# Optimization experiments

Measured on AMD Instinct MI355X. Metric: run time of the kernel, lower is better.

## Reference

```python
import jax, jax.numpy as jnp
import numpy as np

N_NODES = 50000


def _gcn_conv(x, src, dst, W, b, n):
    # PyG GCNConv: h = x @ W; symmetric normalization with self-loops; scatter-add; + bias
    h = x @ W
    deg = jax.ops.segment_sum(jnp.ones_like(dst, dtype=h.dtype), dst, num_segments=n)
    dinv = jax.lax.rsqrt(jnp.maximum(deg, 1.0))  # self-loops guarantee deg >= 1
    norm = dinv[src] * dinv[dst]                 # [E_total]
    msgs = h[src] * norm[:, None]                # gather + scale
    out = jax.ops.segment_sum(msgs, dst, num_segments=n)
    return out + b


def setup_inputs() -> dict:
    key = jax.random.key(0)
    k1, k2, k3, k4 = jax.random.split(key, 4)
    d, f = 128, 128
    x = jax.random.normal(k1, (N_NODES, d), dtype=jnp.float32)
    edge_index = jax.random.randint(k2, (2, 800000), 0, N_NODES, dtype=jnp.int64)
    W1 = jax.random.normal(k3, (d, f), dtype=jnp.float32) / np.sqrt(d)
    b1 = jnp.zeros((f,), dtype=jnp.float32)
    W2 = jax.random.normal(k4, (f, 1), dtype=jnp.float32) / np.sqrt(f)
    b2 = jnp.zeros((1,), dtype=jnp.float32)
    return {"x": x, "edge_index": edge_index, "W1": W1, "b1": b1, "W2": W2, "b2": b2}


def reference(x, edge_index, W1, b1, W2, b2):
    n = x.shape[0]
    loops = jnp.arange(n, dtype=edge_index.dtype)
    src = jnp.concatenate([edge_index[0], loops])
    dst = jnp.concatenate([edge_index[1], loops])
    h = _gcn_conv(x, src, dst, W1, b1, n)
    h = jax.nn.relu(h)
    out = _gcn_conv(h, src, dst, W2, b2, n)
    return out
```

## Files before the change

kernel.cpp:

```cpp
#include <hip/hip_runtime.h>
#include <hip/hip_fp16.h>

#define D 128
#define BINW 64
#define BINCAP 2048
#define SUBT 1568
#define LCAP 48

typedef _Float16 half8 __attribute__((ext_vector_type(8)));
typedef float float4v __attribute__((ext_vector_type(4)));

__global__ __launch_bounds__(256) void fused_bin_gemm_kernel(
    const float* __restrict__ x, const float* __restrict__ W,
    __half* __restrict__ h, const int* __restrict__ idx,
    int* __restrict__ binCount, unsigned* __restrict__ binned,
    int E, int nbin, int n, int SB) {
  __shared__ uint4 smem[2048];
  const int t = threadIdx.x;

  if (blockIdx.x < SB) {
    int*            hist  = (int*)smem;
    int*            cur   = hist + 800;
    unsigned*       recs  = (unsigned*)(cur + 800);
    unsigned short* dbins = (unsigned short*)(recs + SUBT);
    int*            isp   = (int*)(dbins + SUBT);

    for (int b = t; b < 800; b += 256) hist[b] = 0;
    if (t == 0) {
      int any = 0;
      for (int i = 0; i < 64; ++i) any |= idx[2 * i + 1];
      *isp = (any == 0) ? 1 : 0;
    }
    __syncthreads();
    const int is64 = *isp;
    const int lo = blockIdx.x * SUBT;
    const int hi = min(lo + SUBT, E);
    const int cnt_e = hi - lo;

    for (int e = lo + t; e < hi; e += 256) {
      int s, d;
      if (is64) { s = idx[2 * e]; d = idx[2 * (E + e)]; }
      else      { s = idx[e];     d = idx[E + e]; }
      const int li = e - lo;
      const int b = d >> 6;
      recs[li]  = (unsigned)s | ((unsigned)(d & 63) << 16);
      dbins[li] = (unsigned short)b;
      atomicAdd(&hist[b], 1);
    }
    __syncthreads();
    for (int b = t; b < nbin; b += 256) {
      int hv = hist[b];
      cur[b] = hv ? atomicAdd(&binCount[b], hv) : 0;
    }
    __syncthreads();
    for (int li = t; li < cnt_e; li += 256) {
      const int b = dbins[li];
      int pos = atomicAdd(&cur[b], 1);
      pos = min(pos, BINCAP - 1);
      binned[(size_t)b * BINCAP + pos] = recs[li];
    }
  } else {
    const int bid = blockIdx.x - SB;
    uint4 (*bfrag)[4][64] = (uint4(*)[4][64])smem;

    for (int e = t; e < 2048; e += 256) {
      const int nt = e >> 8;
      const int kk = (e >> 6) & 3;
      const int L  = e & 63;
      const int nn = nt * 16 + (L & 15);
      const int k0 = kk * 32 + (L >> 4) * 8;
      half8 v;
#pragma unroll
      for (int j = 0; j < 8; ++j) v[j] = (_Float16)W[(k0 + j) * D + nn];
      bfrag[nt][kk][L] = *(uint4*)&v;
    }
    __syncthreads();

    const int wave = t >> 6;
    const int lane = t & 63;
    const int r0 = bid * 64 + wave * 16;

    const int mrow = r0 + (lane & 15);
    const int mc = (mrow < n) ? mrow : (n - 1);
    half8 af[4];
#pragma unroll
    for (int kk = 0; kk < 4; ++kk) {
      const float* xp = x + (size_t)mc * D + kk * 32 + (lane >> 4) * 8;
      float4 lo4 = *(const float4*)xp;
      float4 hi4 = *(const float4*)(xp + 4);
      half8 v;
      v[0] = (_Float16)lo4.x; v[1] = (_Float16)lo4.y;
      v[2] = (_Float16)lo4.z; v[3] = (_Float16)lo4.w;
      v[4] = (_Float16)hi4.x; v[5] = (_Float16)hi4.y;
      v[6] = (_Float16)hi4.z; v[7] = (_Float16)hi4.w;
      af[kk] = v;
    }

    float4v acc[8];
#pragma unroll
    for (int nt = 0; nt < 8; ++nt) acc[nt] = (float4v){0.f, 0.f, 0.f, 0.f};

#pragma unroll
    for (int nt = 0; nt < 8; ++nt) {
      uint4 b0 = bfrag[nt][0][lane];
      uint4 b1 = bfrag[nt][1][lane];
      uint4 b2 = bfrag[nt][2][lane];
      uint4 b3 = bfrag[nt][3][lane];
      acc[nt] = __builtin_amdgcn_mfma_f32_16x16x32_f16(af[0], *(half8*)&b0, acc[nt], 0, 0, 0);
      acc[nt] = __builtin_amdgcn_mfma_f32_16x16x32_f16(af[1], *(half8*)&b1, acc[nt], 0, 0, 0);
      acc[nt] = __builtin_amdgcn_mfma_f32_16x16x32_f16(af[2], *(half8*)&b2, acc[nt], 0, 0, 0);
      acc[nt] = __builtin_amdgcn_mfma_f32_16x16x32_f16(af[3], *(half8*)&b3, acc[nt], 0, 0, 0);
    }

    __syncthreads();
    __half* hout = (__half*)smem;
    const int quad = lane >> 4;
    const int col  = lane & 15;
    const int rloc = wave * 16 + quad * 4;
#pragma unroll
    for (int r = 0; r < 4; ++r)
#pragma unroll
      for (int nt = 0; nt < 8; ++nt)
        hout[(rloc + r) * D + nt * 16 + col] = __float2half(acc[nt][r]);
    __syncthreads();

    const size_t rowbase = (size_t)bid * 64;
#pragma unroll
    for (int i = 0; i < 4; ++i) {
      const int elt = i * 256 + t;
      const int rr  = elt >> 4;
      if (rowbase + rr < (size_t)n)
        *(uint4*)(h + (rowbase + rr) * D + (elt & 15) * 8) = smem[elt];
    }
  }
}

__global__ __launch_bounds__(256) void sort_lists_kernel(const int* __restrict__ binCount,
                                                         const unsigned* __restrict__ binned,
                                                         unsigned short* __restrict__ lists,
                                                         int* __restrict__ cnt,
                                                         int n, int nbin) {
  __shared__ unsigned rec[BINCAP];
  __shared__ unsigned short srt[BINCAP];
  __shared__ int hist[BINW];
  __shared__ int scn[BINW];
  __shared__ int cur[BINW];
  const int t = threadIdx.x;
  const int b = blockIdx.x;
  int bc = binCount[b];
  if (bc > BINCAP) bc = BINCAP;
  const size_t gbase = (size_t)b * BINCAP;

  for (int i = t; i < bc; i += 256) rec[i] = binned[gbase + i];
  if (t < BINW) hist[t] = 0;
  __syncthreads();
  for (int i = t; i < bc; i += 256) atomicAdd(&hist[rec[i] >> 16], 1);
  __syncthreads();
  if (t < BINW) scn[t] = hist[t];
  __syncthreads();
  for (int off = 1; off < BINW; off <<= 1) {
    int u = 0;
    if (t < BINW && t >= off) u = scn[t - off];
    __syncthreads();
    if (t < BINW) scn[t] += u;
    __syncthreads();
  }
  if (t < BINW) cur[t] = scn[t] - hist[t];
  __syncthreads();
  for (int i = t; i < bc; i += 256) {
    unsigned r = rec[i];
    int pos = atomicAdd(&cur[r >> 16], 1);
    srt[pos] = (unsigned short)(r & 0xFFFFu);
  }
  __syncthreads();
  const int node0 = b * BINW;
  for (int i = t; i < BINW * LCAP; i += 256) {
    const int ln = i / LCAP;
    const int k  = i - ln * LCAP;
    const int node = node0 + ln;
    if (node < n) {
      const int deg = min(hist[ln], LCAP);
      if (k < deg) lists[(size_t)node * LCAP + k] = srt[scn[ln] - hist[ln] + k];
    }
  }
  const int node = node0 + t;
  if (t < BINW && node < n) cnt[node] = hist[t];
}

__device__ __forceinline__ void unpack8(uint4 p, float f[8]) {
  float2 t;
  t = __half22float2(*(__half2*)&p.x); f[0] = t.x; f[1] = t.y;
  t = __half22float2(*(__half2*)&p.y); f[2] = t.x; f[3] = t.y;
  t = __half22float2(*(__half2*)&p.z); f[4] = t.x; f[5] = t.y;
  t = __half22float2(*(__half2*)&p.w); f[6] = t.x; f[7] = t.y;
}

__global__ __launch_bounds__(256) void gather1_kernel(const __half* __restrict__ h,
                                                      const int* __restrict__ cnt,
                                                      const unsigned short* __restrict__ lists,
                                                      const float* __restrict__ b1,
                                                      const float* __restrict__ W2,
                                                      float* __restrict__ zw, int n) {
  const int node = blockIdx.x * 4 + (threadIdx.x >> 6);
  if (node >= n) return;
  const int lane = threadIdx.x & 63;
  const int q    = lane >> 4;
  const int fb   = (lane & 15) * 8;

  const unsigned short* lst = lists + (size_t)node * LCAP;
  const int  c   = cnt[node];
  const int  deg = min(c, LCAP);
  const float di = rsqrtf((float)(c + 1));
  float a[8] = {0.f, 0.f, 0.f, 0.f, 0.f, 0.f, 0.f, 0.f};
  if (q == 0) {
    uint4 p = *(const uint4*)(h + (size_t)node * D + fb);
    float f[8]; unpack8(p, f);
    float s2 = di * di;
#pragma unroll
    for (int k = 0; k < 8; ++k) a[k] = f[k] * s2;
  }

  for (int j = q; j < deg; j += 16) {
    const int j1 = j + 4, j2 = j + 8, j3 = j + 12;
    const bool v1 = j1 < deg, v2 = j2 < deg, v3 = j3 < deg;
    int s0 = lst[j];
    int s1 = v1 ? lst[j1] : s0;
    int s2 = v2 ? lst[j2] : s0;
    int s3 = v3 ? lst[j3] : s0;
    uint4 p0 = *(const uint4*)(h + (size_t)s0 * D + fb);
    uint4 p1 = *(const uint4*)(h + (size_t)s1 * D + fb);
    uint4 p2 = *(const uint4*)(h + (size_t)s2 * D + fb);
    uint4 p3 = *(const uint4*)(h + (size_t)s3 * D + fb);
    float w0 = di * rsqrtf((float)(cnt[s0] + 1));
    float w1 = v1 ? di * rsqrtf((float)(cnt[s1] + 1)) : 0.f;
    float w2 = v2 ? di * rsqrtf((float)(cnt[s2] + 1)) : 0.f;
    float w3 = v3 ? di * rsqrtf((float)(cnt[s3] + 1)) : 0.f;
    float f0[8], f1[8], f2[8], f3[8];
    unpack8(p0, f0); unpack8(p1, f1); unpack8(p2, f2); unpack8(p3, f3);
#pragma unroll
    for (int k = 0; k < 8; ++k) a[k] = fmaf(f0[k], w0, a[k]);
#pragma unroll
    for (int k = 0; k < 8; ++k) a[k] = fmaf(f1[k], w1, a[k]);
#pragma unroll
    for (int k = 0; k < 8; ++k) a[k] = fmaf(f2[k], w2, a[k]);
#pragma unroll
    for (int k = 0; k < 8; ++k) a[k] = fmaf(f3[k], w3, a[k]);
  }

#pragma unroll
  for (int k = 0; k < 8; ++k) {
    a[k] += __shfl_xor(a[k], 16, 64);
    a[k] += __shfl_xor(a[k], 32, 64);
  }

  float4 blo = *(const float4*)(b1 + fb);
  float4 bhi = *(const float4*)(b1 + fb + 4);
  float4 wlo = *(const float4*)(W2 + fb);
  float4 whi = *(const float4*)(W2 + fb + 4);
  float bb[8] = {blo.x, blo.y, blo.z, blo.w, bhi.x, bhi.y, bhi.z, bhi.w};
  float ww[8] = {wlo.x, wlo.y, wlo.z, wlo.w, whi.x, whi.y, whi.z, whi.w};
  float p = 0.f;
#pragma unroll
  for (int k = 0; k < 8; ++k) p += fmaxf(a[k] + bb[k], 0.f) * ww[k];
#pragma unroll
  for (int off = 8; off > 0; off >>= 1) p += __shfl_xor(p, off, 64);
  if (lane == 0) zw[node] = p * di;
}

__global__ __launch_bounds__(256) void gather2_kernel(const float* __restrict__ zw,
                                                      const int* __restrict__ cnt,
                                                      const unsigned short* __restrict__ lists,
                                                      const float* __restrict__ b2,
                                                      float* __restrict__ out, int n) {
  const int node = blockIdx.x * 64 + (threadIdx.x >> 2);
  if (node >= n) return;
  const int l = threadIdx.x & 3;
  const int c = cnt[node];
  const int deg = min(c, LCAP);
  const unsigned short* lst = lists + (size_t)node * LCAP;
  float s = (l == 0) ? zw[node] : 0.f;
  for (int j = l; j < deg; j += 4) s += zw[lst[j]];
  s += __shfl_xor(s, 1, 64);
  s += __shfl_xor(s, 2, 64);
  if (l == 0) out[node] = s * rsqrtf((float)(c + 1)) + b2[0];
}

extern "C" void kernel_launch(void* const* d_in, const int* in_sizes, int n_in,
                              void* d_out, int out_size, void* d_ws, size_t ws_size,
                              hipStream_t stream) {
  const float* x   = (const float*)d_in[0];
  const int*   idx = (const int*)d_in[1];
  const float* W1  = (const float*)d_in[2];
  const float* b1  = (const float*)d_in[3];
  const float* W2  = (const float*)d_in[4];
  const float* b2  = (const float*)d_in[5];
  float* out = (float*)d_out;

  const int n = in_sizes[0] / D;
  const int E = in_sizes[1] / 2;
  const int nbin = (n + BINW - 1) / BINW;

  char* ws = (char*)d_ws;
  size_t off = 0;
  auto carve = [&](size_t bytes) { char* p = ws + off; off += (bytes + 255) & ~(size_t)255; return p; };
  int*            binCount = (int*)carve((size_t)nbin * 4);
  unsigned*       binned   = (unsigned*)carve((size_t)nbin * BINCAP * 4);
  unsigned short* lists    = (unsigned short*)carve((size_t)n * LCAP * 2);
  int*            cnt      = (int*)carve((size_t)n * 4);
  __half*         h        = (__half*)carve((size_t)n * D * 2);
  float*          zw       = (float*)carve((size_t)n * 4);

  const int SB = (E + SUBT - 1) / SUBT;
  const int GB = (n + 63) / 64;

  hipMemsetAsync(binCount, 0, (size_t)nbin * 4, stream);
  fused_bin_gemm_kernel<<<SB + GB, 256, 0, stream>>>(x, W1, h, idx, binCount,
                                                     binned, E, nbin, n, SB);
  sort_lists_kernel<<<nbin, 256, 0, stream>>>(binCount, binned, lists, cnt, n, nbin);
  gather1_kernel<<<(n + 3) / 4, 256, 0, stream>>>(h, cnt, lists, b1, W2, zw, n);
  gather2_kernel<<<(n + 63) / 64, 256, 0, stream>>>(zw, cnt, lists, b2, out, n);
}
```

Before: 160.0 us.

## Switch to two-level binning with coarse 1024-node chunks and coalesced writes

Edges are first binned into 49 coarse chunks of 1024 destination nodes instead of 782 fine bins of 64. Each block locally sorts its records by chunk so it can write contiguous runs to global memory, replacing scattered per-edge writes. The sort kernel then has 16 blocks per chunk; each scans the whole chunk and keeps only records for its 64-node sub-bin. This cuts global atomics and scattered writes, but every chunk is read 16 times and the per-chunk capacity is fixed at 20480 (expected about 16400 edges), so overflow can drop edges.

```diff
diff --git a/kernel.cpp b/kernel.cpp
--- a/kernel.cpp
+++ b/kernel.cpp
@@ -2,6 +2,8 @@
 #include <hip/hip_fp16.h>
 
 #define D 128
+#define NC 64
+#define BINCAP2 20480
 #define BINW 64
 #define BINCAP 2048
 #define SUBT 1568
@@ -13,19 +15,24 @@
 __global__ __launch_bounds__(256) void fused_bin_gemm_kernel(
     const float* __restrict__ x, const float* __restrict__ W,
     __half* __restrict__ h, const int* __restrict__ idx,
-    int* __restrict__ binCount, unsigned* __restrict__ binned,
-    int E, int nbin, int n, int SB) {
+    int* __restrict__ binCount2, unsigned* __restrict__ binned,
+    int E, int nc, int n, int SB) {
   __shared__ uint4 smem[2048];
   const int t = threadIdx.x;
 
   if (blockIdx.x < SB) {
-    int*            hist  = (int*)smem;
-    int*            cur   = hist + 800;
-    unsigned*       recs  = (unsigned*)(cur + 800);
-    unsigned short* dbins = (unsigned short*)(recs + SUBT);
-    int*            isp   = (int*)(dbins + SUBT);
-
-    for (int b = t; b < 800; b += 256) hist[b] = 0;
+    int*           hist  = (int*)smem;
+    int*           scn   = hist + 64;
+    int*           lbase = scn + 64;
+    int*           cur   = lbase + 64;
+    int*           gbase = cur + 64;
+    unsigned*      recs  = (unsigned*)(gbase + 64);
+    unsigned*      srt   = recs + SUBT;
+    unsigned char* dbins = (unsigned char*)(srt + SUBT);
+    unsigned char* sbins = dbins + SUBT;
+    int*           isp   = (int*)(sbins + SUBT);
+
+    if (t < 64) hist[t] = 0;
     if (t == 0) {
       int any = 0;
       for (int i = 0; i < 64; ++i) any |= idx[2 * i + 1];
@@ -42,22 +49,39 @@
       if (is64) { s = idx[2 * e]; d = idx[2 * (E + e)]; }
       else      { s = idx[e];     d = idx[E + e]; }
       const int li = e - lo;
-      const int b = d >> 6;
-      recs[li]  = (unsigned)s | ((unsigned)(d & 63) << 16);
-      dbins[li] = (unsigned short)b;
+      const int b = d >> 10;
+      recs[li]  = (unsigned)s | ((unsigned)(d & 1023) << 16);
+      dbins[li] = (unsigned char)b;
       atomicAdd(&hist[b], 1);
     }
     __syncthreads();
-    for (int b = t; b < nbin; b += 256) {
-      int hv = hist[b];
-      cur[b] = hv ? atomicAdd(&binCount[b], hv) : 0;
+    if (t < 64) scn[t] = hist[t];
+    __syncthreads();
+    for (int off = 1; off < 64; off <<= 1) {
+      int u = 0;
+      if (t < 64 && t >= off) u = scn[t - off];
+      __syncthreads();
+      if (t < 64) scn[t] += u;
+      __syncthreads();
+    }
+    if (t < 64) {
+      lbase[t] = scn[t] - hist[t];
+      cur[t]   = scn[t] - hist[t];
+      gbase[t] = (t < nc && hist[t]) ? atomicAdd(&binCount2[t], hist[t]) : 0;
     }
     __syncthreads();
     for (int li = t; li < cnt_e; li += 256) {
       const int b = dbins[li];
-      int pos = atomicAdd(&cur[b], 1);
-      pos = min(pos, BINCAP - 1);
-      binned[(size_t)b * BINCAP + pos] = recs[li];
+      const int slot = atomicAdd(&cur[b], 1);
+      srt[slot]  = recs[li];
+      sbins[slot] = (unsigned char)b;
+    }
+    __syncthreads();
+    for (int i = t; i < cnt_e; i += 256) {
+      const int b = sbins[i];
+      const int pos = gbase[b] + (i - lbase[b]);
+      if (pos < BINCAP2)
+        binned[(size_t)b * BINCAP2 + pos] = srt[i];
     }
   } else {
     const int bid = blockIdx.x - SB;
@@ -135,26 +159,37 @@
   }
 }
 
-__global__ __launch_bounds__(256) void sort_lists_kernel(const int* __restrict__ binCount,
+__global__ __launch_bounds__(256) void sort_lists_kernel(const int* __restrict__ binCount2,
                                                          const unsigned* __restrict__ binned,
                                                          unsigned short* __restrict__ lists,
                                                          int* __restrict__ cnt,
-                                                         int n, int nbin) {
+                                                         int n, int nc) {
   __shared__ unsigned rec[BINCAP];
   __shared__ unsigned short srt[BINCAP];
   __shared__ int hist[BINW];
   __shared__ int scn[BINW];
   __shared__ int cur[BINW];
+  __shared__ int nloc;
   const int t = threadIdx.x;
-  const int b = blockIdx.x;
-  int bc = binCount[b];
-  if (bc > BINCAP) bc = BINCAP;
-  const size_t gbase = (size_t)b * BINCAP;
-
-  for (int i = t; i < bc; i += 256) rec[i] = binned[gbase + i];
+  const int f = blockIdx.x;
+  const int c = f >> 4;
+  const int sub = f & 15;
+  const int bc2 = min(binCount2[c], BINCAP2);
+  const size_t cbase = (size_t)c * BINCAP2;
+
+  if (t == 0) nloc = 0;
   if (t < BINW) hist[t] = 0;
   __syncthreads();
-  for (int i = t; i < bc; i += 256) atomicAdd(&hist[rec[i] >> 16], 1);
+  for (int i = t; i < bc2; i += 256) {
+    const unsigned r = binned[cbase + i];
+    if (((r >> 22) & 15u) == (unsigned)sub) {
+      const int p = atomicAdd(&nloc, 1);
+      if (p < BINCAP) rec[p] = r;
+    }
+  }
+  __syncthreads();
+  const int bc = min(nloc, BINCAP);
+  for (int i = t; i < bc; i += 256) atomicAdd(&hist[(rec[i] >> 16) & 63u], 1);
   __syncthreads();
   if (t < BINW) scn[t] = hist[t];
   __syncthreads();
@@ -168,12 +203,12 @@
   if (t < BINW) cur[t] = scn[t] - hist[t];
   __syncthreads();
   for (int i = t; i < bc; i += 256) {
-    unsigned r = rec[i];
-    int pos = atomicAdd(&cur[r >> 16], 1);
+    const unsigned r = rec[i];
+    const int pos = atomicAdd(&cur[(r >> 16) & 63u], 1);
     srt[pos] = (unsigned short)(r & 0xFFFFu);
   }
   __syncthreads();
-  const int node0 = b * BINW;
+  const int node0 = f * BINW;
   for (int i = t; i < BINW * LCAP; i += 256) {
     const int ln = i / LCAP;
     const int k  = i - ln * LCAP;
@@ -298,25 +333,26 @@
 
   const int n = in_sizes[0] / D;
   const int E = in_sizes[1] / 2;
+  const int nc   = (n + 1023) >> 10;
   const int nbin = (n + BINW - 1) / BINW;
 
   char* ws = (char*)d_ws;
   size_t off = 0;
   auto carve = [&](size_t bytes) { char* p = ws + off; off += (bytes + 255) & ~(size_t)255; return p; };
-  int*            binCount = (int*)carve((size_t)nbin * 4);
-  unsigned*       binned   = (unsigned*)carve((size_t)nbin * BINCAP * 4);
-  unsigned short* lists    = (unsigned short*)carve((size_t)n * LCAP * 2);
-  int*            cnt      = (int*)carve((size_t)n * 4);
-  __half*         h        = (__half*)carve((size_t)n * D * 2);
-  float*          zw       = (float*)carve((size_t)n * 4);
+  int*            binCount2 = (int*)carve((size_t)NC * 4);
+  unsigned*       binned    = (unsigned*)carve((size_t)NC * BINCAP2 * 4);
+  unsigned short* lists     = (unsigned short*)carve((size_t)n * LCAP * 2);
+  int*            cnt       = (int*)carve((size_t)n * 4);
+  __half*         h         = (__half*)carve((size_t)n * D * 2);
+  float*          zw        = (float*)carve((size_t)n * 4);
 
   const int SB = (E + SUBT - 1) / SUBT;
   const int GB = (n + 63) / 64;
 
-  hipMemsetAsync(binCount, 0, (size_t)nbin * 4, stream);
-  fused_bin_gemm_kernel<<<SB + GB, 256, 0, stream>>>(x, W1, h, idx, binCount,
-                                                     binned, E, nbin, n, SB);
-  sort_lists_kernel<<<nbin, 256, 0, stream>>>(binCount, binned, lists, cnt, n, nbin);
+  hipMemsetAsync(binCount2, 0, (size_t)NC * 4, stream);
+  fused_bin_gemm_kernel<<<SB + GB, 256, 0, stream>>>(x, W1, h, idx, binCount2,
+                                                     binned, E, nc, n, SB);
+  sort_lists_kernel<<<nbin, 256, 0, stream>>>(binCount2, binned, lists, cnt, n, nc);
   gather1_kernel<<<(n + 3) / 4, 256, 0, stream>>>(h, cnt, lists, b1, W2, zw, n);
   gather2_kernel<<<(n + 63) / 64, 256, 0, stream>>>(zw, cnt, lists, b2, out, n);
 }
```

After: 174.7 us. 1.09x slower.
